# Kernel optimization log

Measured on AMD Instinct MI355X. Metric: run time of the kernel, lower is better.

## Reference

```python
import jax, jax.numpy as jnp
import numpy as np

N_NODES = 100000
N_EDGES = 1600000
IN_FEATS = 256
OUT_FEATS = 256


def setup_inputs() -> dict:
    key = jax.random.key(0)
    k1, k2, k3, k4, k5, k6, k7, k8 = jax.random.split(key, 8)
    stdv = 1.0 / np.sqrt(OUT_FEATS)
    inp = {
        "h": jax.random.normal(k1, (N_NODES, IN_FEATS), dtype=jnp.float32),
        "norm": jax.random.uniform(k2, (N_NODES, 1), dtype=jnp.float32),
        "src": jax.random.randint(k3, (N_EDGES,), 0, N_NODES, dtype=jnp.int32),
        "dst": jax.random.randint(k4, (N_EDGES,), 0, N_NODES, dtype=jnp.int32),
        # GCN weight: uniform(-stdv, stdv) as in reset_parameters
        "weight": jax.random.uniform(k5, (IN_FEATS, OUT_FEATS), dtype=jnp.float32,
                                     minval=-stdv, maxval=stdv),
        "bias": jax.random.uniform(k6, (OUT_FEATS,), dtype=jnp.float32,
                                   minval=-stdv, maxval=stdv),
        # residual 1x1 Conv1d: weight [out, in] (kernel size 1 squeezed), bias zeros
        "res_w": jax.random.normal(k7, (OUT_FEATS, IN_FEATS), dtype=jnp.float32)
                 * np.sqrt(2.0 / OUT_FEATS),
        "res_b": jnp.zeros((OUT_FEATS,), dtype=jnp.float32),
    }
    return inp


def reference(h, norm, src, dst, weight, bias, res_w, res_b):
    # h: [N, F_in], norm: [N, 1]
    hw = (h @ weight) * norm                      # [N, F_out]
    # copy_src + sum over edges: gather from src, scatter-add to dst
    agg = jax.ops.segment_sum(hw[src], dst, num_segments=N_NODES)  # [N, F_out]
    agg = agg * norm + bias
    # residual path: 1x1 Conv1d over channel dim == linear per node
    res = h @ res_w.T + res_b                     # [N, F_out]
    return jax.nn.relu(agg + res)
```

## Files before the change

kernel.cpp:

```cpp
#include <hip/hip_runtime.h>

#define N_NODES 100000
#define N_EDGES 1600000
#define FEAT 256
#define KTOT 512
#define NBUCK ((N_NODES + 63) / 64)
#define SEGN (NBUCK * 8)

typedef __attribute__((ext_vector_type(8))) short short8v;
typedef __attribute__((ext_vector_type(4))) float f32x4;
typedef __attribute__((ext_vector_type(4))) unsigned short ushort4v;

__device__ __forceinline__ unsigned short f2bf(float f) {
    unsigned u = __float_as_uint(f);
    return (unsigned short)((u + 0x7FFFu + ((u >> 16) & 1u)) >> 16);
}
__device__ __forceinline__ float bf2f(unsigned short s) {
    return __uint_as_float(((unsigned)s) << 16);
}
__device__ __forceinline__ short8v zero8() {
    short8v v;
    #pragma unroll
    for (int i = 0; i < 8; ++i) v[i] = 0;
    return v;
}

constexpr size_t OFF_XH   = 0;
constexpr size_t XH_BYTES = (size_t)N_NODES * KTOT * 2;
constexpr size_t OFF_BT   = XH_BYTES;
constexpr size_t OFF_SEGC = OFF_BT + 262144;
constexpr size_t OFF_SEGB = OFF_SEGC + 51200;
constexpr size_t OFF_SEGU = OFF_SEGB + 51200;
constexpr size_t OFF_OFFS = OFF_SEGU + 51200;
constexpr size_t OFF_CSR  = OFF_OFFS + 400384;
constexpr size_t WS_NEEDED = OFF_CSR + (size_t)N_EDGES * 4;

__device__ __forceinline__ int seg_of(int d) {
    return ((d >> 6) << 3) | (d & 7);
}

__global__ __launch_bounds__(256) void cast_h_kernel(
    const float* __restrict__ h, unsigned short* __restrict__ xh)
{
    int tid = blockIdx.x * 256 + threadIdx.x;
    int row = tid >> 5;
    int c8  = (tid & 31) * 8;
    const float4* p = (const float4*)&h[(size_t)row * FEAT + c8];
    float4 a = p[0], b = p[1];
    unsigned short tmp[8];
    tmp[0]=f2bf(a.x); tmp[1]=f2bf(a.y); tmp[2]=f2bf(a.z); tmp[3]=f2bf(a.w);
    tmp[4]=f2bf(b.x); tmp[5]=f2bf(b.y); tmp[6]=f2bf(b.z); tmp[7]=f2bf(b.w);
    *(short8v*)&xh[(size_t)row * KTOT + 256 + c8] = *(short8v*)tmp;
}

__global__ __launch_bounds__(256) void prep_b_kernel(
    const float* __restrict__ W, const float* __restrict__ res_w,
    unsigned short* __restrict__ Bt)
{
    int n = blockIdx.x, t = threadIdx.x;
    Bt[(size_t)n * KTOT + t]       = f2bf(W[(size_t)t * FEAT + n]);
    Bt[(size_t)n * KTOT + 256 + t] = f2bf(res_w[(size_t)n * FEAT + t]);
}

__global__ __launch_bounds__(256) void count_kernel(
    const int* __restrict__ dst, int* __restrict__ segc)
{
    int e = blockIdx.x * 256 + threadIdx.x;
    if (e < N_EDGES) atomicAdd(&segc[seg_of(dst[e])], 1);
}

__global__ __launch_bounds__(1024) void scan_seg_kernel(
    const int* __restrict__ segc,
    int* __restrict__ segb, int* __restrict__ segu)
{
    __shared__ int part[1024];
    const int t = threadIdx.x;
    const int C = (SEGN + 1023) / 1024;
    const int lo = t * C;
    const int hi = min(lo + C, SEGN);
    int s = 0;
    for (int i = lo; i < hi; ++i) s += segc[i];
    part[t] = s;
    __syncthreads();
    for (int d = 1; d < 1024; d <<= 1) {
        int u = (t >= d) ? part[t - d] : 0;
        __syncthreads();
        part[t] += u;
        __syncthreads();
    }
    int prefix = part[t] - s;
    for (int i = lo; i < hi; ++i) {
        int c = segc[i];
        segb[i] = prefix;
        segu[i] = prefix;
        prefix += c;
    }
    if (t == 0) segb[SEGN] = N_EDGES;
}

__global__ __launch_bounds__(256) void bin_kernel(
    const int* __restrict__ src, const int* __restrict__ dst,
    int* __restrict__ segu, unsigned int* __restrict__ bin)
{
    int e = blockIdx.x * 256 + threadIdx.x;
    if (e < N_EDGES) {
        int d = dst[e];
        int p = atomicAdd(&segu[seg_of(d)], 1);
        bin[p] = ((unsigned)(d & 63) << 20) | (unsigned)src[e];
    }
}

__global__ __launch_bounds__(256) void sortcsr_kernel(
    const unsigned int* __restrict__ bin,
    const int* __restrict__ segb,
    int* __restrict__ csr, int* __restrict__ offs)
{
    __shared__ int cnt64[64];
    __shared__ int base64[64];
    __shared__ int cur64[64];
    const int b = blockIdx.x, t = threadIdx.x;
    const int lo = segb[b * 8];
    const int hi = segb[b * 8 + 8];
    if (t < 64) cnt64[t] = 0;
    __syncthreads();
    for (int e = lo + t; e < hi; e += 256)
        atomicAdd(&cnt64[bin[e] >> 20], 1);
    __syncthreads();
    if (t == 0) {
        int acc = 0;
        for (int i = 0; i < 64; ++i) { base64[i] = acc; acc += cnt64[i]; }
    }
    __syncthreads();
    if (t < 64) {
        int o = lo + base64[t];
        offs[b * 64 + t] = o;
        cur64[t] = o;
    }
    __syncthreads();
    for (int e = lo + t; e < hi; e += 256) {
        unsigned pk = bin[e];
        int p = atomicAdd(&cur64[pk >> 20], 1);
        csr[p] = (int)(pk & 0xFFFFF);
    }
}

__global__ __launch_bounds__(256) void aggregate_kernel(
    const float* __restrict__ norm,
    const int*   __restrict__ offs,
    const int*   __restrict__ csr_src,
    unsigned short* __restrict__ xh)
{
    const int wave = threadIdx.x >> 6;
    const int lane = threadIdx.x & 63;
    const int n    = blockIdx.x * 4 + wave;
    if (n >= N_NODES) return;
    const int start = offs[n];
    const int end   = offs[n + 1];
    float a0=0,a1=0,a2=0,a3=0, b0=0,b1=0,b2=0,b3=0;
    int e = start;
    for (; e + 1 < end; e += 2) {
        int s0 = csr_src[e];
        int s1 = csr_src[e + 1];
        float m0 = norm[s0], m1 = norm[s1];
        ushort4v v0 = *(const ushort4v*)&xh[(size_t)s0 * KTOT + 256 + lane * 4];
        ushort4v v1 = *(const ushort4v*)&xh[(size_t)s1 * KTOT + 256 + lane * 4];
        a0 = fmaf(bf2f(v0.x), m0, a0); a1 = fmaf(bf2f(v0.y), m0, a1);
        a2 = fmaf(bf2f(v0.z), m0, a2); a3 = fmaf(bf2f(v0.w), m0, a3);
        b0 = fmaf(bf2f(v1.x), m1, b0); b1 = fmaf(bf2f(v1.y), m1, b1);
        b2 = fmaf(bf2f(v1.z), m1, b2); b3 = fmaf(bf2f(v1.w), m1, b3);
    }
    if (e < end) {
        int s0 = csr_src[e];
        float m0 = norm[s0];
        ushort4v v0 = *(const ushort4v*)&xh[(size_t)s0 * KTOT + 256 + lane * 4];
        a0 = fmaf(bf2f(v0.x), m0, a0); a1 = fmaf(bf2f(v0.y), m0, a1);
        a2 = fmaf(bf2f(v0.z), m0, a2); a3 = fmaf(bf2f(v0.w), m0, a3);
    }
    float nm = norm[n];
    unsigned short tmp[4];
    tmp[0] = f2bf((a0 + b0) * nm);
    tmp[1] = f2bf((a1 + b1) * nm);
    tmp[2] = f2bf((a2 + b2) * nm);
    tmp[3] = f2bf((a3 + b3) * nm);
    *(ushort4v*)&xh[(size_t)n * KTOT + lane * 4] = *(ushort4v*)tmp;
}

#define GBM 128
#define GBN 128
#define GBK 32
#define LDT 40

__global__ __launch_bounds__(256) void mfma_gemm_kernel(
    const unsigned short* __restrict__ xh,
    const unsigned short* __restrict__ Bt,
    const float* __restrict__ bias,
    const float* __restrict__ res_b,
    float* __restrict__ out)
{
    __shared__ unsigned short As[GBM * LDT];
    __shared__ unsigned short Bs[GBN * LDT];
    const int t    = threadIdx.x;
    const int m0   = blockIdx.x * GBM;
    const int n0   = blockIdx.y * GBN;
    const int wave = t >> 6, lane = t & 63;
    const int wm   = wave >> 1, wn = wave & 1;
    const int lrow = lane & 15, kg = lane >> 4;

    f32x4 zf = {0.f, 0.f, 0.f, 0.f};
    f32x4 acc[4][4];
    #pragma unroll
    for (int i = 0; i < 4; ++i)
        #pragma unroll
        for (int j = 0; j < 4; ++j) acc[i][j] = zf;

    for (int k0 = 0; k0 < KTOT; k0 += GBK) {
        #pragma unroll
        for (int it = 0; it < 2; ++it) {
            int idx = it * 256 + t;
            int row = idx >> 2;
            int ch  = (idx & 3) * 8;
            int grow = m0 + row;
            short8v va = zero8();
            if (grow < N_NODES)
                va = *(const short8v*)&xh[(size_t)grow * KTOT + k0 + ch];
            *(short8v*)&As[row * LDT + ch] = va;
            short8v vb = *(const short8v*)&Bt[(size_t)(n0 + row) * KTOT + k0 + ch];
            *(short8v*)&Bs[row * LDT + ch] = vb;
        }
        __syncthreads();

        short8v af[4], bfr[4];
        #pragma unroll
        for (int i = 0; i < 4; ++i) {
            af[i]  = *(const short8v*)&As[(wm * 64 + i * 16 + lrow) * LDT + kg * 8];
            bfr[i] = *(const short8v*)&Bs[(wn * 64 + i * 16 + lrow) * LDT + kg * 8];
        }
        #pragma unroll
        for (int i = 0; i < 4; ++i)
            #pragma unroll
            for (int j = 0; j < 4; ++j)
                acc[i][j] = __builtin_amdgcn_mfma_f32_16x16x32_bf16(
                    af[i], bfr[j], acc[i][j], 0, 0, 0);
        __syncthreads();
    }

    #pragma unroll
    for (int j = 0; j < 4; ++j) {
        int col = n0 + wn * 64 + j * 16 + lrow;
        float bb = bias[col] + res_b[col];
        #pragma unroll
        for (int i = 0; i < 4; ++i) {
            int rbase = m0 + wm * 64 + i * 16 + kg * 4;
            #pragma unroll
            for (int r = 0; r < 4; ++r) {
                int row = rbase + r;
                if (row < N_NODES)
                    out[(size_t)row * FEAT + col] = fmaxf(acc[i][j][r] + bb, 0.f);
            }
        }
    }
}

#define BM 64
#define BN 64
#define BK 64
#define LDSS 68

template<int MODE>
__global__ __launch_bounds__(256) void gemm_kernel(
    const float* __restrict__ A, const float* __restrict__ B,
    const float* __restrict__ norm, const float* __restrict__ bias,
    const float* __restrict__ res_b, const float* __restrict__ agg,
    float* __restrict__ C)
{
    __shared__ float A_T[BK][LDSS];
    __shared__ float B_s[BK][LDSS];
    const int t = threadIdx.x;
    const int m0 = blockIdx.x * BM, n0 = blockIdx.y * BN;
    const int tx = t & 15, ty = t >> 4;
    float acc[4][4] = {};
    for (int k0 = 0; k0 < FEAT; k0 += BK) {
        #pragma unroll
        for (int i = 0; i < 4; ++i) {
            int idx = i * 256 + t;
            int m = idx >> 4, k4 = (idx & 15) * 4;
            int row = m0 + m;
            float4 v = make_float4(0.f,0.f,0.f,0.f);
            if (row < N_NODES) v = *(const float4*)&A[(size_t)row * FEAT + k0 + k4];
            A_T[k4+0][m]=v.x; A_T[k4+1][m]=v.y; A_T[k4+2][m]=v.z; A_T[k4+3][m]=v.w;
        }
        #pragma unroll
        for (int i = 0; i < 4; ++i) {
            int idx = i * 256 + t;
            if (MODE == 0) {
                int k = idx >> 4, n4 = (idx & 15) * 4;
                *(float4*)&B_s[k][n4] = *(const float4*)&B[(size_t)(k0+k)*FEAT + n0 + n4];
            } else {
                int n = idx >> 4, k4 = (idx & 15) * 4;
                float4 v = *(const float4*)&B[(size_t)(n0+n)*FEAT + k0 + k4];
                B_s[k4+0][n]=v.x; B_s[k4+1][n]=v.y; B_s[k4+2][n]=v.z; B_s[k4+3][n]=v.w;
            }
        }
        __syncthreads();
        #pragma unroll
        for (int kk = 0; kk < BK; ++kk) {
            float4 av = *(const float4*)&A_T[kk][ty*4];
            float4 bv = *(const float4*)&B_s[kk][tx*4];
            const float a[4]={av.x,av.y,av.z,av.w}, b[4]={bv.x,bv.y,bv.z,bv.w};
            #pragma unroll
            for (int i=0;i<4;++i)
                #pragma unroll
                for (int j=0;j<4;++j) acc[i][j]=fmaf(a[i],b[j],acc[i][j]);
        }
        __syncthreads();
    }
    if (MODE == 0) {
        #pragma unroll
        for (int i=0;i<4;++i) {
            int row=m0+ty*4+i;
            if (row<N_NODES) {
                float nm=norm[row];
                float4 o; o.x=acc[i][0]*nm; o.y=acc[i][1]*nm; o.z=acc[i][2]*nm; o.w=acc[i][3]*nm;
                *(float4*)&C[(size_t)row*FEAT+n0+tx*4]=o;
            }
        }
    } else {
        float4 bv=*(const float4*)&bias[n0+tx*4];
        float4 rb=*(const float4*)&res_b[n0+tx*4];
        #pragma unroll
        for (int i=0;i<4;++i) {
            int row=m0+ty*4+i;
            if (row<N_NODES) {
                float nm=norm[row];
                float4 ag=*(const float4*)&agg[(size_t)row*FEAT+n0+tx*4];
                float4 o;
                o.x=fmaxf(fmaf(ag.x,nm,bv.x)+acc[i][0]+rb.x,0.f);
                o.y=fmaxf(fmaf(ag.y,nm,bv.y)+acc[i][1]+rb.y,0.f);
                o.z=fmaxf(fmaf(ag.z,nm,bv.z)+acc[i][2]+rb.z,0.f);
                o.w=fmaxf(fmaf(ag.w,nm,bv.w)+acc[i][3]+rb.w,0.f);
                *(float4*)&C[(size_t)row*FEAT+n0+tx*4]=o;
            }
        }
    }
}

__global__ __launch_bounds__(256) void scatter_kernel(
    const float* __restrict__ hw, const int* __restrict__ src,
    const int* __restrict__ dst, float* __restrict__ agg)
{
    const int t = threadIdx.x;
    const int e0 = blockIdx.x * 8;
    #pragma unroll
    for (int i = 0; i < 8; ++i) {
        int e = e0 + i;
        if (e < N_EDGES) {
            int s = src[e], d = dst[e];
            atomicAdd(&agg[(size_t)d * FEAT + t], hw[(size_t)s * FEAT + t]);
        }
    }
}

extern "C" void kernel_launch(void* const* d_in, const int* in_sizes, int n_in,
                              void* d_out, int out_size, void* d_ws, size_t ws_size,
                              hipStream_t stream) {
    const float* h      = (const float*)d_in[0];
    const float* norm   = (const float*)d_in[1];
    const int*   src    = (const int*)d_in[2];
    const int*   dst    = (const int*)d_in[3];
    const float* weight = (const float*)d_in[4];
    const float* bias   = (const float*)d_in[5];
    const float* res_w  = (const float*)d_in[6];
    const float* res_b  = (const float*)d_in[7];
    float* out = (float*)d_out;
    char* ws = (char*)d_ws;

    if (ws_size >= WS_NEEDED) {
        unsigned short* xh = (unsigned short*)(ws + OFF_XH);
        unsigned short* Bt = (unsigned short*)(ws + OFF_BT);
        int* segc = (int*)(ws + OFF_SEGC);
        int* segb = (int*)(ws + OFF_SEGB);
        int* segu = (int*)(ws + OFF_SEGU);
        int* offs = (int*)(ws + OFF_OFFS);
        int* csr  = (int*)(ws + OFF_CSR);
        unsigned int* bin = (unsigned int*)d_out;

        cast_h_kernel<<<N_NODES * FEAT / 8 / 256, 256, 0, stream>>>(h, xh);
        prep_b_kernel<<<256, 256, 0, stream>>>(weight, res_w, Bt);
        hipMemsetAsync(segc, 0, 51200, stream);
        count_kernel<<<(N_EDGES + 255) / 256, 256, 0, stream>>>(dst, segc);
        scan_seg_kernel<<<1, 1024, 0, stream>>>(segc, segb, segu);
        bin_kernel<<<(N_EDGES + 255) / 256, 256, 0, stream>>>(src, dst, segu, bin);
        sortcsr_kernel<<<NBUCK, 256, 0, stream>>>(bin, segb, csr, offs);
        aggregate_kernel<<<(N_NODES + 3) / 4, 256, 0, stream>>>(norm, offs, csr, xh);
        dim3 gg((N_NODES + GBM - 1) / GBM, FEAT / GBN);
        mfma_gemm_kernel<<<gg, 256, 0, stream>>>(xh, Bt, bias, res_b, out);
    } else {
        float* hw = (float*)ws;
        dim3 gdim((N_NODES + BM - 1) / BM, FEAT / BN);
        gemm_kernel<0><<<gdim, 256, 0, stream>>>(h, weight, norm, nullptr, nullptr, nullptr, hw);
        hipMemsetAsync(out, 0, (size_t)N_NODES * FEAT * sizeof(float), stream);
        scatter_kernel<<<N_EDGES / 8, 256, 0, stream>>>(hw, src, dst, out);
        gemm_kernel<1><<<gdim, 256, 0, stream>>>(h, res_w, norm, bias, res_b, out, out);
    }
}
```

Baseline: 581.0 us.

## Fuse prep kernels, parallelize segment scan, unroll aggregation, widen GEMM tile

Merges the h cast, edge count and weight-prep kernels into one launch split by block id. Replaces the single-block segment scan with a three-pass multi-block scan. Unrolls the aggregation loop to four independent accumulators so more gathers are in flight. Widens the MFMA GEMM tile to cover all 256 output columns per block, so each A tile is loaded once, at the cost of more accumulator registers and possibly lower occupancy.

New measurement: 567.9 us. 1.02x faster.

```diff
diff --git a/kernel.cpp b/kernel.cpp
--- a/kernel.cpp
+++ b/kernel.cpp
@@ -6,6 +6,9 @@
 #define KTOT 512
 #define NBUCK ((N_NODES + 63) / 64)
 #define SEGN (NBUCK * 8)
+#define CAST_BLOCKS 12500
+#define COUNT_BLOCKS 6250
+#define SCANB 13
 
 typedef __attribute__((ext_vector_type(8))) short short8v;
 typedef __attribute__((ext_vector_type(4))) float f32x4;
@@ -32,55 +35,73 @@
 constexpr size_t OFF_SEGB = OFF_SEGC + 51200;
 constexpr size_t OFF_SEGU = OFF_SEGB + 51200;
 constexpr size_t OFF_OFFS = OFF_SEGU + 51200;
-constexpr size_t OFF_CSR  = OFF_OFFS + 400384;
+constexpr size_t OFF_BSUM = OFF_OFFS + 400384;
+constexpr size_t OFF_CSR  = OFF_BSUM + 1024;
 constexpr size_t WS_NEEDED = OFF_CSR + (size_t)N_EDGES * 4;
 
 __device__ __forceinline__ int seg_of(int d) {
     return ((d >> 6) << 3) | (d & 7);
 }
 
-__global__ __launch_bounds__(256) void cast_h_kernel(
-    const float* __restrict__ h, unsigned short* __restrict__ xh)
-{
-    int tid = blockIdx.x * 256 + threadIdx.x;
-    int row = tid >> 5;
-    int c8  = (tid & 31) * 8;
-    const float4* p = (const float4*)&h[(size_t)row * FEAT + c8];
-    float4 a = p[0], b = p[1];
-    unsigned short tmp[8];
-    tmp[0]=f2bf(a.x); tmp[1]=f2bf(a.y); tmp[2]=f2bf(a.z); tmp[3]=f2bf(a.w);
-    tmp[4]=f2bf(b.x); tmp[5]=f2bf(b.y); tmp[6]=f2bf(b.z); tmp[7]=f2bf(b.w);
-    *(short8v*)&xh[(size_t)row * KTOT + 256 + c8] = *(short8v*)tmp;
-}
-
-__global__ __launch_bounds__(256) void prep_b_kernel(
-    const float* __restrict__ W, const float* __restrict__ res_w,
-    unsigned short* __restrict__ Bt)
-{
-    int n = blockIdx.x, t = threadIdx.x;
-    Bt[(size_t)n * KTOT + t]       = f2bf(W[(size_t)t * FEAT + n]);
-    Bt[(size_t)n * KTOT + 256 + t] = f2bf(res_w[(size_t)n * FEAT + t]);
-}
-
-__global__ __launch_bounds__(256) void count_kernel(
-    const int* __restrict__ dst, int* __restrict__ segc)
-{
-    int e = blockIdx.x * 256 + threadIdx.x;
-    if (e < N_EDGES) atomicAdd(&segc[seg_of(dst[e])], 1);
-}
-
-__global__ __launch_bounds__(1024) void scan_seg_kernel(
-    const int* __restrict__ segc,
+__global__ __launch_bounds__(256) void prep_count_kernel(
+    const float* __restrict__ h, const float* __restrict__ W,
+    const float* __restrict__ res_w, const int* __restrict__ dst,
+    unsigned short* __restrict__ xh, unsigned short* __restrict__ Bt,
+    int* __restrict__ segc)
+{
+    const int bid = blockIdx.x, t = threadIdx.x;
+    if (bid < CAST_BLOCKS) {
+        int tid = bid * 256 + t;
+        int row = tid >> 5;
+        int c8  = (tid & 31) * 8;
+        const float4* p = (const float4*)&h[(size_t)row * FEAT + c8];
+        float4 a = p[0], b = p[1];
+        unsigned short tmp[8];
+        tmp[0]=f2bf(a.x); tmp[1]=f2bf(a.y); tmp[2]=f2bf(a.z); tmp[3]=f2bf(a.w);
+        tmp[4]=f2bf(b.x); tmp[5]=f2bf(b.y); tmp[6]=f2bf(b.z); tmp[7]=f2bf(b.w);
+        *(short8v*)&xh[(size_t)row * KTOT + 256 + c8] = *(short8v*)tmp;
+    } else if (bid < CAST_BLOCKS + COUNT_BLOCKS) {
+        int e = (bid - CAST_BLOCKS) * 256 + t;
+        atomicAdd(&segc[seg_of(dst[e])], 1);
+    } else {
+        int n = bid - (CAST_BLOCKS + COUNT_BLOCKS);
+        Bt[(size_t)n * KTOT + t]       = f2bf(W[(size_t)t * FEAT + n]);
+        Bt[(size_t)n * KTOT + 256 + t] = f2bf(res_w[(size_t)n * FEAT + t]);
+    }
+}
+
+__global__ __launch_bounds__(1024) void segscan_p1(
+    const int* __restrict__ segc, int* __restrict__ bsum)
+{
+    __shared__ int red[1024];
+    int i = blockIdx.x * 1024 + threadIdx.x;
+    red[threadIdx.x] = (i < SEGN) ? segc[i] : 0;
+    __syncthreads();
+    #pragma unroll
+    for (int d = 512; d > 0; d >>= 1) {
+        if (threadIdx.x < d) red[threadIdx.x] += red[threadIdx.x + d];
+        __syncthreads();
+    }
+    if (threadIdx.x == 0) bsum[blockIdx.x] = red[0];
+}
+
+__global__ __launch_bounds__(64) void segscan_p2(int* __restrict__ bsum)
+{
+    if (threadIdx.x == 0) {
+        int acc = 0;
+        for (int i = 0; i < SCANB; ++i) { int c = bsum[i]; bsum[i] = acc; acc += c; }
+    }
+}
+
+__global__ __launch_bounds__(1024) void segscan_p3(
+    const int* __restrict__ segc, const int* __restrict__ bsum,
     int* __restrict__ segb, int* __restrict__ segu)
 {
     __shared__ int part[1024];
-    const int t = threadIdx.x;
-    const int C = (SEGN + 1023) / 1024;
-    const int lo = t * C;
-    const int hi = min(lo + C, SEGN);
-    int s = 0;
-    for (int i = lo; i < hi; ++i) s += segc[i];
-    part[t] = s;
+    const int b = blockIdx.x, t = threadIdx.x;
+    const int i = b * 1024 + t;
+    int v = (i < SEGN) ? segc[i] : 0;
+    part[t] = v;
     __syncthreads();
     for (int d = 1; d < 1024; d <<= 1) {
         int u = (t >= d) ? part[t - d] : 0;
@@ -88,14 +109,9 @@
         part[t] += u;
         __syncthreads();
     }
-    int prefix = part[t] - s;
-    for (int i = lo; i < hi; ++i) {
-        int c = segc[i];
-        segb[i] = prefix;
-        segu[i] = prefix;
-        prefix += c;
-    }
-    if (t == 0) segb[SEGN] = N_EDGES;
+    int ex = bsum[b] + part[t] - v;
+    if (i < SEGN) { segb[i] = ex; segu[i] = ex; }
+    if (i == SEGN) segb[SEGN] = N_EDGES;
 }
 
 __global__ __launch_bounds__(256) void bin_kernel(
@@ -156,20 +172,28 @@
     if (n >= N_NODES) return;
     const int start = offs[n];
     const int end   = offs[n + 1];
-    float a0=0,a1=0,a2=0,a3=0, b0=0,b1=0,b2=0,b3=0;
+    float a0=0,a1=0,a2=0,a3=0;
+    float b0=0,b1=0,b2=0,b3=0;
+    float c0=0,c1=0,c2=0,c3=0;
+    float d0=0,d1=0,d2=0,d3=0;
     int e = start;
-    for (; e + 1 < end; e += 2) {
-        int s0 = csr_src[e];
-        int s1 = csr_src[e + 1];
-        float m0 = norm[s0], m1 = norm[s1];
+    for (; e + 3 < end; e += 4) {
+        int s0 = csr_src[e], s1 = csr_src[e+1], s2 = csr_src[e+2], s3 = csr_src[e+3];
+        float m0 = norm[s0], m1 = norm[s1], m2 = norm[s2], m3 = norm[s3];
         ushort4v v0 = *(const ushort4v*)&xh[(size_t)s0 * KTOT + 256 + lane * 4];
         ushort4v v1 = *(const ushort4v*)&xh[(size_t)s1 * KTOT + 256 + lane * 4];
+        ushort4v v2 = *(const ushort4v*)&xh[(size_t)s2 * KTOT + 256 + lane * 4];
+        ushort4v v3 = *(const ushort4v*)&xh[(size_t)s3 * KTOT + 256 + lane * 4];
         a0 = fmaf(bf2f(v0.x), m0, a0); a1 = fmaf(bf2f(v0.y), m0, a1);
         a2 = fmaf(bf2f(v0.z), m0, a2); a3 = fmaf(bf2f(v0.w), m0, a3);
         b0 = fmaf(bf2f(v1.x), m1, b0); b1 = fmaf(bf2f(v1.y), m1, b1);
         b2 = fmaf(bf2f(v1.z), m1, b2); b3 = fmaf(bf2f(v1.w), m1, b3);
-    }
-    if (e < end) {
+        c0 = fmaf(bf2f(v2.x), m2, c0); c1 = fmaf(bf2f(v2.y), m2, c1);
+        c2 = fmaf(bf2f(v2.z), m2, c2); c3 = fmaf(bf2f(v2.w), m2, c3);
+        d0 = fmaf(bf2f(v3.x), m3, d0); d1 = fmaf(bf2f(v3.y), m3, d1);
+        d2 = fmaf(bf2f(v3.z), m3, d2); d3 = fmaf(bf2f(v3.w), m3, d3);
+    }
+    for (; e < end; ++e) {
         int s0 = csr_src[e];
         float m0 = norm[s0];
         ushort4v v0 = *(const ushort4v*)&xh[(size_t)s0 * KTOT + 256 + lane * 4];
@@ -178,15 +202,15 @@
     }
     float nm = norm[n];
     unsigned short tmp[4];
-    tmp[0] = f2bf((a0 + b0) * nm);
-    tmp[1] = f2bf((a1 + b1) * nm);
-    tmp[2] = f2bf((a2 + b2) * nm);
-    tmp[3] = f2bf((a3 + b3) * nm);
+    tmp[0] = f2bf(((a0 + b0) + (c0 + d0)) * nm);
+    tmp[1] = f2bf(((a1 + b1) + (c1 + d1)) * nm);
+    tmp[2] = f2bf(((a2 + b2) + (c2 + d2)) * nm);
+    tmp[3] = f2bf(((a3 + b3) + (c3 + d3)) * nm);
     *(ushort4v*)&xh[(size_t)n * KTOT + lane * 4] = *(ushort4v*)tmp;
 }
 
 #define GBM 128
-#define GBN 128
+#define GBN2 256
 #define GBK 32
 #define LDT 40
 
@@ -198,20 +222,19 @@
     float* __restrict__ out)
 {
     __shared__ unsigned short As[GBM * LDT];
-    __shared__ unsigned short Bs[GBN * LDT];
+    __shared__ unsigned short Bs[GBN2 * LDT];
     const int t    = threadIdx.x;
     const int m0   = blockIdx.x * GBM;
-    const int n0   = blockIdx.y * GBN;
     const int wave = t >> 6, lane = t & 63;
     const int wm   = wave >> 1, wn = wave & 1;
     const int lrow = lane & 15, kg = lane >> 4;
 
     f32x4 zf = {0.f, 0.f, 0.f, 0.f};
-    f32x4 acc[4][4];
+    f32x4 acc[4][8];
     #pragma unroll
     for (int i = 0; i < 4; ++i)
         #pragma unroll
-        for (int j = 0; j < 4; ++j) acc[i][j] = zf;
+        for (int j = 0; j < 8; ++j) acc[i][j] = zf;
 
     for (int k0 = 0; k0 < KTOT; k0 += GBK) {
         #pragma unroll
@@ -224,29 +247,36 @@
             if (grow < N_NODES)
                 va = *(const short8v*)&xh[(size_t)grow * KTOT + k0 + ch];
             *(short8v*)&As[row * LDT + ch] = va;
-            short8v vb = *(const short8v*)&Bt[(size_t)(n0 + row) * KTOT + k0 + ch];
+        }
+        #pragma unroll
+        for (int it = 0; it < 4; ++it) {
+            int idx = it * 256 + t;
+            int row = idx >> 2;
+            int ch  = (idx & 3) * 8;
+            short8v vb = *(const short8v*)&Bt[(size_t)row * KTOT + k0 + ch];
             *(short8v*)&Bs[row * LDT + ch] = vb;
         }
         __syncthreads();
 
-        short8v af[4], bfr[4];
-        #pragma unroll
-        for (int i = 0; i < 4; ++i) {
-            af[i]  = *(const short8v*)&As[(wm * 64 + i * 16 + lrow) * LDT + kg * 8];
-            bfr[i] = *(const short8v*)&Bs[(wn * 64 + i * 16 + lrow) * LDT + kg * 8];
-        }
+        short8v af[4], bfr[8];
+        #pragma unroll
+        for (int i = 0; i < 4; ++i)
+            af[i] = *(const short8v*)&As[(wm * 64 + i * 16 + lrow) * LDT + kg * 8];
+        #pragma unroll
+        for (int j = 0; j < 8; ++j)
+            bfr[j] = *(const short8v*)&Bs[(wn * 128 + j * 16 + lrow) * LDT + kg * 8];
         #pragma unroll
         for (int i = 0; i < 4; ++i)
             #pragma unroll
-            for (int j = 0; j < 4; ++j)
+            for (int j = 0; j < 8; ++j)
                 acc[i][j] = __builtin_amdgcn_mfma_f32_16x16x32_bf16(
                     af[i], bfr[j], acc[i][j], 0, 0, 0);
         __syncthreads();
     }
 
     #pragma unroll
-    for (int j = 0; j < 4; ++j) {
-        int col = n0 + wn * 64 + j * 16 + lrow;
+    for (int j = 0; j < 8; ++j) {
+        int col = wn * 128 + j * 16 + lrow;
         float bb = bias[col] + res_b[col];
         #pragma unroll
         for (int i = 0; i < 4; ++i) {
@@ -381,19 +411,21 @@
         int* segb = (int*)(ws + OFF_SEGB);
         int* segu = (int*)(ws + OFF_SEGU);
         int* offs = (int*)(ws + OFF_OFFS);
+        int* bsum = (int*)(ws + OFF_BSUM);
         int* csr  = (int*)(ws + OFF_CSR);
         unsigned int* bin = (unsigned int*)d_out;
 
-        cast_h_kernel<<<N_NODES * FEAT / 8 / 256, 256, 0, stream>>>(h, xh);
-        prep_b_kernel<<<256, 256, 0, stream>>>(weight, res_w, Bt);
         hipMemsetAsync(segc, 0, 51200, stream);
-        count_kernel<<<(N_EDGES + 255) / 256, 256, 0, stream>>>(dst, segc);
-        scan_seg_kernel<<<1, 1024, 0, stream>>>(segc, segb, segu);
+        prep_count_kernel<<<CAST_BLOCKS + COUNT_BLOCKS + 256, 256, 0, stream>>>(
+            h, weight, res_w, dst, xh, Bt, segc);
+        segscan_p1<<<SCANB, 1024, 0, stream>>>(segc, bsum);
+        segscan_p2<<<1, 64, 0, stream>>>(bsum);
+        segscan_p3<<<SCANB, 1024, 0, stream>>>(segc, bsum, segb, segu);
         bin_kernel<<<(N_EDGES + 255) / 256, 256, 0, stream>>>(src, dst, segu, bin);
         sortcsr_kernel<<<NBUCK, 256, 0, stream>>>(bin, segb, csr, offs);
         aggregate_kernel<<<(N_NODES + 3) / 4, 256, 0, stream>>>(norm, offs, csr, xh);
-        dim3 gg((N_NODES + GBM - 1) / GBM, FEAT / GBN);
-        mfma_gemm_kernel<<<gg, 256, 0, stream>>>(xh, Bt, bias, res_b, out);
+        mfma_gemm_kernel<<<(N_NODES + GBM - 1) / GBM, 256, 0, stream>>>(
+            xh, Bt, bias, res_b, out);
     } else {
         float* hw = (float*)ws;
         dim3 gdim((N_NODES + BM - 1) / BM, FEAT / BN);
```
